# Kernel tuning notes

Hardware: AMD Instinct MI355X
Metric: run time of the kernel (lower is better)

## Reference

```python
import jax, jax.numpy as jnp
import numpy as np


def setup_inputs() -> dict:
    key = jax.random.key(0)
    ks = jax.random.split(key, 11)
    B, E, R, D = 2048, 20000, 500, 256
    inp = {
        "h": jax.random.uniform(ks[0], (B, E), dtype=jnp.float32),
        "t": jax.random.uniform(ks[1], (B, E), dtype=jnp.float32),
        "r": jax.random.uniform(ks[2], (B, R), dtype=jnp.float32),
        "W_er": jax.random.normal(ks[3], (D, E), dtype=jnp.float32) * 0.02,
        "W_ei": jax.random.normal(ks[4], (D, E), dtype=jnp.float32) * 0.02,
        "W_ej": jax.random.normal(ks[5], (D, E), dtype=jnp.float32) * 0.02,
        "W_ek": jax.random.normal(ks[6], (D, E), dtype=jnp.float32) * 0.02,
        "W_rr": jax.random.normal(ks[7], (D, R), dtype=jnp.float32) * 0.02,
        "W_ri": jax.random.normal(ks[8], (D, R), dtype=jnp.float32) * 0.02,
        "W_rj": jax.random.normal(ks[9], (D, R), dtype=jnp.float32) * 0.02,
        "W_rk": jax.random.normal(ks[10], (D, R), dtype=jnp.float32) * 0.02,
    }
    return inp


def reference(h, t, r, W_er, W_ei, W_ej, W_ek, W_rr, W_ri, W_rj, W_rk):
    # entity / relation projections (nn.Linear, no bias): x @ W^T -> [B, D]
    H_r, H_i, H_j, H_k = h @ W_er.T, h @ W_ei.T, h @ W_ej.T, h @ W_ek.T
    T_r, T_i, T_j, T_k = t @ W_er.T, t @ W_ei.T, t @ W_ej.T, t @ W_ek.T
    R_r, R_i, R_j, R_k = r @ W_rr.T, r @ W_ri.T, r @ W_rj.T, r @ W_rk.T

    # hypercomplex norm per row: sqrt(|R_r|^2 + |R_i|^2 + |R_j|^2 + |R_k|^2) -> [B,1]
    norm = jnp.sqrt(
        jnp.sum(R_r * R_r + R_i * R_i + R_j * R_j + R_k * R_k, axis=1, keepdims=True)
    )
    R_r, R_i, R_j, R_k = norm * R_r, norm * R_i, norm * R_j, norm * R_k

    # Hamilton product H (x) R
    Q_r = H_r * R_r - H_i * R_i - H_j * R_j - H_k * R_k
    Q_i = H_r * R_i + H_i * R_r + H_j * R_k - H_k * R_j
    Q_j = H_r * R_j - H_i * R_k + H_j * R_r + H_k * R_i
    Q_k = H_r * R_k + H_i * R_j - H_j * R_i + H_k * R_r

    # diag(Q @ T^T) == rowwise dot sum(Q*T, axis=1) -- O(B*d) form of the anti-pattern
    score = jnp.sum(Q_r * T_r + Q_i * T_i + Q_j * T_j + Q_k * T_k, axis=1, keepdims=True)
    return jax.nn.sigmoid(score)
```

## Files before the change

### kernel.cpp

```cpp
#include <hip/hip_runtime.h>


using bf16x8 = __attribute__((ext_vector_type(8))) short;
using f32x4  = __attribute__((ext_vector_type(4))) float;
using f32x16 = __attribute__((ext_vector_type(16))) float;

#define DEVINL static __device__ __forceinline__

DEVINL void split2(float x0, float x1, unsigned& h, unsigned& l) {
  unsigned u0 = __float_as_uint(x0), u1 = __float_as_uint(x1);
  unsigned h0 = u0 & 0xFFFF0000u, h1 = u1 & 0xFFFF0000u;
  h = (u0 >> 16) | h1;
  float r0 = x0 - __uint_as_float(h0);
  float r1 = x1 - __uint_as_float(h1);
  l = (__float_as_uint(r0) >> 16) | (__float_as_uint(r1) & 0xFFFF0000u);
}

DEVINL void gload16(const void* g, void* l) {
  __builtin_amdgcn_global_load_lds(
      (const __attribute__((address_space(1))) unsigned*)g,
      (__attribute__((address_space(3))) unsigned*)l, 16, 0, 0);
}

__global__ void convert_img(const float* __restrict__ src0,
                            const float* __restrict__ src1, int rows0,
                            int srcK, char* __restrict__ dst, int ktiles)
{
  const int kt = blockIdx.x, rt = blockIdx.y;
  const int m  = threadIdx.x;
  const int row = rt * 256 + m;
  const float* srow = (row < rows0) ? (src0 + (size_t)row * srcK)
                                    : (src1 + (size_t)(row - rows0) * srcK);
  char* base = dst + ((size_t)rt * ktiles + kt) * 32768
             + (m >> 5) * 2048 + (m & 31) * 16;
#pragma unroll
  for (int oct = 0; oct < 4; ++oct) {
    int k0 = kt * 32 + oct * 8;
    float x[8];
    if (k0 + 8 <= srcK) {
      float4 v0 = *(const float4*)(srow + k0);
      float4 v1 = *(const float4*)(srow + k0 + 4);
      x[0] = v0.x; x[1] = v0.y; x[2] = v0.z; x[3] = v0.w;
      x[4] = v1.x; x[5] = v1.y; x[6] = v1.z; x[7] = v1.w;
    } else {
#pragma unroll
      for (int j = 0; j < 8; ++j) x[j] = (k0 + j < srcK) ? srow[k0 + j] : 0.f;
    }
    unsigned hh[4], ll[4];
    split2(x[0], x[1], hh[0], ll[0]);
    split2(x[2], x[3], hh[1], ll[1]);
    split2(x[4], x[5], hh[2], ll[2]);
    split2(x[6], x[7], hh[3], ll[3]);
    int off = (oct >> 1) * 1024 + (oct & 1) * 512;
    *(uint4*)(base + off)         = make_uint4(hh[0], hh[1], hh[2], hh[3]);
    *(uint4*)(base + 16384 + off) = make_uint4(ll[0], ll[1], ll[2], ll[3]);
  }
}

__global__ __launch_bounds__(512, 2) void gemm_img(
    const char* __restrict__ Aimg, const char* __restrict__ Bimg, int ktiles,
    float* __restrict__ C, int MT, int NT, int KS, int swz)
{
  __shared__ __align__(16) char smem[131072];
  const int tid = threadIdx.x;
  const int bid = blockIdx.x;

  int mt, nt, ks;
  if (swz) {
    int x = bid & 7, w = bid >> 3;
    nt = w & 3;
    int g = x + (w >> 2) * 8;
    mt = g & 15; ks = g >> 4;
  } else {
    nt = bid % NT; int q = bid / NT; mt = q % MT; ks = q / MT;
  }

  const int kt0 = (ktiles * ks) / KS;
  const int kt1 = (ktiles * (ks + 1)) / KS;

  const char* Ab = Aimg + ((size_t)mt * ktiles + kt0) * 32768;
  const char* Bb = Bimg + ((size_t)nt * ktiles + kt0) * 32768;

  const int wid = tid >> 6, lane = tid & 63;
  const int wr = wid >> 2, wc = wid & 3;

  f32x16 acc[4][2];
#pragma unroll
  for (int mb = 0; mb < 4; ++mb)
#pragma unroll
    for (int nb = 0; nb < 2; ++nb)
#pragma unroll
      for (int e = 0; e < 16; ++e) acc[mb][nb][e] = 0.f;

  {
    const char* As = Ab + wid * 4096 + lane * 16;
    const char* Bs = Bb + wid * 4096 + lane * 16;
#pragma unroll
    for (int i = 0; i < 4; ++i) gload16(As + i * 1024, smem + wid * 4096 + i * 1024);
#pragma unroll
    for (int i = 0; i < 4; ++i) gload16(Bs + i * 1024, smem + 32768 + wid * 4096 + i * 1024);
  }
  asm volatile("s_waitcnt vmcnt(0)" ::: "memory");
  __builtin_amdgcn_s_barrier();

  for (int kt = kt0; kt < kt1; ++kt) {
    char* bufc = smem + (size_t)((kt - kt0) & 1) * 65536;
    char* bufn = smem + (size_t)(((kt - kt0) & 1) ^ 1) * 65536;
    const bool nx = (kt + 1 < kt1);

    if (nx) {
      const char* As = Ab + (size_t)(kt + 1 - kt0) * 32768 + wid * 4096 + lane * 16;
      const char* Bs = Bb + (size_t)(kt + 1 - kt0) * 32768 + wid * 4096 + lane * 16;
#pragma unroll
      for (int i = 0; i < 4; ++i) gload16(As + i * 1024, bufn + wid * 4096 + i * 1024);
#pragma unroll
      for (int i = 0; i < 4; ++i) gload16(Bs + i * 1024, bufn + 32768 + wid * 4096 + i * 1024);
    }

    bf16x8 bh[2][2], bl[2][2];
#pragma unroll
    for (int nb = 0; nb < 2; ++nb)
#pragma unroll
      for (int s = 0; s < 2; ++s) {
        const char* p = bufc + 32768 + (wc * 2 + nb) * 2048 + s * 1024 + lane * 16;
        bh[nb][s] = *(const bf16x8*)p;
        bl[nb][s] = *(const bf16x8*)(p + 16384);
      }

    __builtin_amdgcn_s_setprio(1);
#pragma unroll
    for (int mb = 0; mb < 4; ++mb) {
      const char* p = bufc + (wr * 4 + mb) * 2048 + lane * 16;
      bf16x8 ah0 = *(const bf16x8*)(p);
      bf16x8 al0 = *(const bf16x8*)(p + 16384);
      bf16x8 ah1 = *(const bf16x8*)(p + 1024);
      bf16x8 al1 = *(const bf16x8*)(p + 1024 + 16384);
#pragma unroll
      for (int nb = 0; nb < 2; ++nb) {
        f32x16* a = &acc[mb][nb];
        *a = __builtin_amdgcn_mfma_f32_32x32x16_bf16(ah0, bh[nb][0], *a, 0, 0, 0);
        *a = __builtin_amdgcn_mfma_f32_32x32x16_bf16(al0, bh[nb][0], *a, 0, 0, 0);
        *a = __builtin_amdgcn_mfma_f32_32x32x16_bf16(ah0, bl[nb][0], *a, 0, 0, 0);
        *a = __builtin_amdgcn_mfma_f32_32x32x16_bf16(ah1, bh[nb][1], *a, 0, 0, 0);
        *a = __builtin_amdgcn_mfma_f32_32x32x16_bf16(al1, bh[nb][1], *a, 0, 0, 0);
        *a = __builtin_amdgcn_mfma_f32_32x32x16_bf16(ah1, bl[nb][1], *a, 0, 0, 0);
      }
    }
    __builtin_amdgcn_s_setprio(0);

    asm volatile("s_waitcnt vmcnt(0)" ::: "memory");
    __builtin_amdgcn_s_barrier();
  }

  float* Cb = C + (size_t)ks * (size_t)(MT * 256) * 1024;
  const long rowbase = (long)mt * 256 + wr * 128 + 4 * (lane >> 5);
  const long colbase = (long)nt * 256 + wc * 64 + (lane & 31);
#pragma unroll
  for (int mb = 0; mb < 4; ++mb)
#pragma unroll
    for (int nb = 0; nb < 2; ++nb)
#pragma unroll
      for (int reg = 0; reg < 16; ++reg) {
        long row = rowbase + mb * 32 + (reg & 3) + 8 * (reg >> 2);
        long col = colbase + nb * 32;
        Cb[(size_t)row * 1024 + col] = acc[mb][nb][reg];
      }
}

__global__ void convert_b16(const float* __restrict__ src, int srcK,
                            char* __restrict__ dst)
{
  const int tile = blockIdx.x;
  const int wrow = threadIdx.x;
  char* base = dst + (size_t)tile * 32768;
  const float* srow = src + (size_t)wrow * srcK;
#pragma unroll
  for (int kc8 = 0; kc8 < 4; ++kc8) {
    int k0 = tile * 32 + kc8 * 8;
    float x[8];
    if (k0 + 8 <= srcK) {
      float4 v0 = *(const float4*)(srow + k0);
      float4 v1 = *(const float4*)(srow + k0 + 4);
      x[0] = v0.x; x[1] = v0.y; x[2] = v0.z; x[3] = v0.w;
      x[4] = v1.x; x[5] = v1.y; x[6] = v1.z; x[7] = v1.w;
    } else {
#pragma unroll
      for (int j = 0; j < 8; ++j) x[j] = (k0 + j < srcK) ? srow[k0 + j] : 0.f;
    }
    unsigned hh[4], ll[4];
    split2(x[0], x[1], hh[0], ll[0]);
    split2(x[2], x[3], hh[1], ll[1]);
    split2(x[4], x[5], hh[2], ll[2]);
    split2(x[6], x[7], hh[3], ll[3]);
    int lchunk = (wrow & 15) + kc8 * 16;
    int n16 = wrow >> 4;
    *(uint4*)(base + (size_t)n16 * 1024 + lchunk * 16)         = make_uint4(hh[0], hh[1], hh[2], hh[3]);
    *(uint4*)(base + 16384 + (size_t)n16 * 1024 + lchunk * 16) = make_uint4(ll[0], ll[1], ll[2], ll[3]);
  }
}

__global__ void pad_r(const float* __restrict__ src, float* __restrict__ dst)
{
  int row = blockIdx.y;
  int k = threadIdx.x * 4;
  float4 v = make_float4(0.f, 0.f, 0.f, 0.f);
  if (k + 3 < 500) v = *(const float4*)(src + (size_t)row * 500 + k);
  *(float4*)(dst + (size_t)row * 512 + k) = v;
}

__global__ __launch_bounds__(512, 2) void gemm3p(
    const float* __restrict__ A0, const float* __restrict__ A1, int mtA0, long lda,
    const char* __restrict__ Bimg, int ktilesTot,
    float* __restrict__ C, long ldc, int MT, int NT, int KS, int swz)
{
  extern __shared__ char smemd[];
  const int tid = threadIdx.x;
  const int bid = blockIdx.x;

  int mt, nt, ks;
  if (swz) {
    int x = bid & 7, w = bid >> 3;
    nt = w & 3;
    int g = x + (w >> 2) * 8;
    mt = g & 15; ks = g >> 4;
  } else {
    nt = bid % NT; int q = bid / NT; mt = q % MT; ks = q / MT;
  }

  const int kt0 = (ktilesTot * ks) / KS;
  const int kt1 = (ktilesTot * (ks + 1)) / KS;

  const float* Ablk = (mt < mtA0) ? (A0 + (size_t)mt * 256 * lda)
                                  : (A1 + (size_t)(mt - mtA0) * 256 * lda);
  const char* Bt = Bimg + ((size_t)nt * ktilesTot + kt0) * 32768;

  const int wid = tid >> 6, lane = tid & 63;
  const int wr = wid >> 2, wc = wid & 3;
  const int l15 = lane & 15, lq = lane >> 4;

  const float* aSrc = Ablk + (size_t)(wid * 32 + (lane >> 3)) * lda
                      + (size_t)kt0 * 32 + 4 * (lane & 7);

  int awoff[4];
  {
    int kg = (lane & 7) >> 1, half = lane & 1;
#pragma unroll
    for (int i = 0; i < 4; ++i) {
      int m15 = (lane >> 3) + 8 * (i & 1);
      awoff[i] = (2 * wid + (i >> 1)) * 2048 + (((m15 ^ kg) + kg * 16) << 4) + half * 8;
    }
  }
  const int aroff = (((l15 ^ lq) + lq * 16) << 4);
  const int bbase = 32768 + (wc * 4) * 1024 + lane * 16;

  f32x4 acc[8][4];
#pragma unroll
  for (int m = 0; m < 8; ++m)
#pragma unroll
    for (int j = 0; j < 4; ++j)
#pragma unroll
      for (int e = 0; e < 4; ++e) acc[m][j][e] = 0.f;

  float4 aR[4];

#define ISSUE_A(KT)                                                            \
  {                                                                            \
    const float* p_ = aSrc + (size_t)((KT) - kt0) * 32;                        \
    _Pragma("unroll")                                                          \
    for (int i = 0; i < 4; ++i) aR[i] = *(const float4*)(p_ + (size_t)(8 * i) * lda); \
  }
#define ISSUE_B(DST, KT)                                                       \
  {                                                                            \
    const char* p_ = Bt + (size_t)((KT) - kt0) * 32768 + wid * 4096 + lane * 16; \
    _Pragma("unroll")                                                          \
    for (int i = 0; i < 4; ++i)                                                \
      gload16(p_ + i * 1024, (DST) + 32768 + wid * 4096 + i * 1024);           \
  }
#define WRITE_A(DST)                                                           \
  {                                                                            \
    _Pragma("unroll")                                                          \
    for (int i = 0; i < 4; ++i) {                                              \
      unsigned h0_, l0_, h1_, l1_;                                             \
      split2(aR[i].x, aR[i].y, h0_, l0_);                                      \
      split2(aR[i].z, aR[i].w, h1_, l1_);                                      \
      *(uint2*)((DST) + awoff[i])        = make_uint2(h0_, h1_);               \
      *(uint2*)((DST) + awoff[i] + 1024) = make_uint2(l0_, l1_);               \
    }                                                                          \
  }

  ISSUE_A(kt0);
  ISSUE_B(smemd, kt0);
  WRITE_A(smemd);
  asm volatile("s_waitcnt vmcnt(0)" ::: "memory");
  asm volatile("s_waitcnt lgkmcnt(0)" ::: "memory");
  __builtin_amdgcn_s_barrier();

  for (int kt = kt0; kt < kt1; ++kt) {
    char* bufc = smemd + (size_t)((kt - kt0) & 1) * 65536;
    char* bufn = smemd + (size_t)(((kt - kt0) & 1) ^ 1) * 65536;
    const bool nx = (kt + 1 < kt1);

    if (nx) { ISSUE_A(kt + 1); ISSUE_B(bufn, kt + 1); }

    bf16x8 bh[4], bl[4];
#pragma unroll
    for (int j = 0; j < 4; ++j) {
      bh[j] = *(const bf16x8*)(bufc + bbase + j * 1024);
      bl[j] = *(const bf16x8*)(bufc + bbase + j * 1024 + 16384);
    }

    __builtin_amdgcn_s_setprio(1);
#pragma unroll
    for (int m = 0; m < 4; ++m) {
      const char* ab = bufc + (wr * 8 + m) * 2048;
      bf16x8 ah = *(const bf16x8*)(ab + aroff);
      bf16x8 al = *(const bf16x8*)(ab + aroff + 1024);
#pragma unroll
      for (int j = 0; j < 4; ++j) {
        acc[m][j] = __builtin_amdgcn_mfma_f32_16x16x32_bf16(ah, bh[j], acc[m][j], 0, 0, 0);
        acc[m][j] = __builtin_amdgcn_mfma_f32_16x16x32_bf16(al, bh[j], acc[m][j], 0, 0, 0);
        acc[m][j] = __builtin_amdgcn_mfma_f32_16x16x32_bf16(ah, bl[j], acc[m][j], 0, 0, 0);
      }
    }
    __builtin_amdgcn_s_setprio(0);

    __builtin_amdgcn_sched_barrier(0);
    if (nx) WRITE_A(bufn);

    __builtin_amdgcn_s_setprio(1);
#pragma unroll
    for (int m = 4; m < 8; ++m) {
      const char* ab = bufc + (wr * 8 + m) * 2048;
      bf16x8 ah = *(const bf16x8*)(ab + aroff);
      bf16x8 al = *(const bf16x8*)(ab + aroff + 1024);
#pragma unroll
      for (int j = 0; j < 4; ++j) {
        acc[m][j] = __builtin_amdgcn_mfma_f32_16x16x32_bf16(ah, bh[j], acc[m][j], 0, 0, 0);
        acc[m][j] = __builtin_amdgcn_mfma_f32_16x16x32_bf16(al, bh[j], acc[m][j], 0, 0, 0);
        acc[m][j] = __builtin_amdgcn_mfma_f32_16x16x32_bf16(ah, bl[j], acc[m][j], 0, 0, 0);
      }
    }
    __builtin_amdgcn_s_setprio(0);

    asm volatile("s_waitcnt vmcnt(0)" ::: "memory");
    asm volatile("s_waitcnt lgkmcnt(0)" ::: "memory");
    __builtin_amdgcn_s_barrier();
  }
#undef ISSUE_A
#undef ISSUE_B
#undef WRITE_A

  float* Cb = C + (size_t)ks * (size_t)(MT * 256) * (size_t)ldc;
  const long rowbase = (long)mt * 256 + wr * 128 + lq * 4;
  const long colbase = (long)nt * 256 + wc * 64 + l15;
#pragma unroll
  for (int m = 0; m < 8; ++m)
#pragma unroll
    for (int j = 0; j < 4; ++j)
#pragma unroll
      for (int reg = 0; reg < 4; ++reg) {
        long row = rowbase + m * 16 + reg;
        long col = colbase + j * 16;
        Cb[(size_t)row * ldc + col] = acc[m][j][reg];
      }
}

__global__ void epilogue_kernel(const float* __restrict__ C1, const float* __restrict__ C2,
                                float* __restrict__ out, int KS)
{
  const int b = blockIdx.x;
  const int d = threadIdx.x;
  const size_t SZ = 4096ull * 1024ull;

  float Hq[4], Tq[4], Rq[4];
#pragma unroll
  for (int q = 0; q < 4; ++q) {
    float hv = 0.f, tv = 0.f;
    for (int ks = 0; ks < KS; ++ks) {
      hv += C1[ks * SZ + (size_t)b * 1024 + q * 256 + d];
      tv += C1[ks * SZ + (size_t)(b + 2048) * 1024 + q * 256 + d];
    }
    Hq[q] = hv; Tq[q] = tv;
    Rq[q] = C2[(size_t)b * 1024 + q * 256 + d];
  }
  float nn = Rq[0]*Rq[0] + Rq[1]*Rq[1] + Rq[2]*Rq[2] + Rq[3]*Rq[3];
  float Qr = Hq[0]*Rq[0] - Hq[1]*Rq[1] - Hq[2]*Rq[2] - Hq[3]*Rq[3];
  float Qi = Hq[0]*Rq[1] + Hq[1]*Rq[0] + Hq[2]*Rq[3] - Hq[3]*Rq[2];
  float Qj = Hq[0]*Rq[2] - Hq[1]*Rq[3] + Hq[2]*Rq[0] + Hq[3]*Rq[1];
  float Qk = Hq[0]*Rq[3] + Hq[1]*Rq[2] - Hq[2]*Rq[1] + Hq[3]*Rq[0];
  float ss = Qr*Tq[0] + Qi*Tq[1] + Qj*Tq[2] + Qk*Tq[3];

#pragma unroll
  for (int o = 32; o; o >>= 1) {
    ss += __shfl_xor(ss, o);
    nn += __shfl_xor(nn, o);
  }
  __shared__ float red[8];
  int lane = d & 63, w = d >> 6;
  if (lane == 0) { red[w] = ss; red[4 + w] = nn; }
  __syncthreads();
  if (d == 0) {
    float S = red[0] + red[1] + red[2] + red[3];
    float N = red[4] + red[5] + red[6] + red[7];
    float score = sqrtf(N) * S;
    out[b] = 1.f / (1.f + expf(-score));
  }
}

extern "C" void kernel_launch(void* const* d_in, const int* in_sizes, int n_in,
                              void* d_out, int out_size, void* d_ws, size_t ws_size,
                              hipStream_t stream)
{
  const float* h = (const float*)d_in[0];
  const float* t = (const float*)d_in[1];
  const float* r = (const float*)d_in[2];
  const float* We[4] = {(const float*)d_in[3], (const float*)d_in[4],
                        (const float*)d_in[5], (const float*)d_in[6]};
  const float* Wr[4] = {(const float*)d_in[7], (const float*)d_in[8],
                        (const float*)d_in[9], (const float*)d_in[10]};
  float* out = (float*)d_out;
  char* ws = (char*)d_ws;

  const size_t offA  = 0;
  const size_t offB  = 327680000;
  const size_t offWr = offB + 81920000;
  const size_t offRi = offWr + 2097152;
  const size_t offC1 = offRi + 4194304;
  const size_t C1sz  = 4096ull * 1024ull * 4ull;
  const size_t offC2 = offC1 + 4 * C1sz;
  const size_t needImg = offC2 + 8388608;

  if (ws_size >= needImg) {
    float* C1 = (float*)(ws + offC1);
    float* C2 = (float*)(ws + offC2);

    convert_img<<<dim3(625, 16), 256, 0, stream>>>(h, t, 2048, 20000, ws + offA, 625);
    for (int q = 0; q < 4; ++q) {
      convert_img<<<dim3(625, 1), 256, 0, stream>>>(
          We[q], We[q], 2048, 20000, ws + offB + (size_t)q * 625 * 32768, 625);
      convert_img<<<dim3(16, 1), 256, 0, stream>>>(
          Wr[q], Wr[q], 2048, 500, ws + offWr + (size_t)q * 16 * 32768, 16);
    }
    convert_img<<<dim3(16, 8), 256, 0, stream>>>(r, r, 4096, 500, ws + offRi, 16);

    gemm_img<<<dim3(256), 512, 0, stream>>>(
        ws + offA, ws + offB, 625, C1, 16, 4, 4, 1);
    gemm_img<<<dim3(32), 512, 0, stream>>>(
        ws + offRi, ws + offWr, 16, C2, 8, 4, 1, 0);

    epilogue_kernel<<<dim3(2048), 256, 0, stream>>>(C1, C2, out, 4);
    return;
  }

  const size_t fB  = 0;
  const size_t fWr = 81920000;
  const size_t fR  = fWr + 2097152;
  const size_t fC1 = fR + 4194304;
  const int KS = (ws_size >= fC1 + 4 * C1sz + 8388608ull) ? 4 : 2;
  const size_t fC2 = fC1 + (size_t)KS * C1sz;

  float* rpad = (float*)(ws + fR);
  float* C1   = (float*)(ws + fC1);
  float* C2   = (float*)(ws + fC2);

  for (int q = 0; q < 4; ++q) {
    convert_b16<<<dim3(625), 256, 0, stream>>>(We[q], 20000, ws + fB + (size_t)q * 625 * 32768);
    convert_b16<<<dim3(16), 256, 0, stream>>>(Wr[q], 500, ws + fWr + (size_t)q * 16 * 32768);
  }
  pad_r<<<dim3(1, 2048), 128, 0, stream>>>(r, rpad);

  gemm3p<<<dim3(16 * 4 * KS), 512, 131072, stream>>>(
      h, t, 8, 20000L, (const char*)(ws + fB), 625,
      C1, 1024L, 16, 4, KS, KS == 4 ? 1 : 0);
  gemm3p<<<dim3(32), 512, 131072, stream>>>(
      rpad, rpad, 8, 512L, (const char*)(ws + fWr), 16,
      C2, 1024L, 8, 4, 1, 0);

  epilogue_kernel<<<dim3(2048), 256, 0, stream>>>(C1, C2, out, KS);
}
```

Before: 690.1 us.

## Switch GEMM to 128-row tiles with single-buffered LDS and 4 waves

Rewrites the split-bf16 GEMM kernel to use 128x256 output tiles with 256 threads and a single 64KB LDS buffer instead of 256x256 tiles with 512 threads and double buffering. The convert kernel is parameterised by row tile so the A image matches the 128-row layout, and the grid grows to 512 blocks. It also prefetches A fragments from LDS ahead of the MFMA loop with sched barriers. The aims are more blocks for occupancy and lower LDS per block, at the cost of no global-load/compute overlap and less data reuse per tile.

```diff
diff --git a/kernel.cpp b/kernel.cpp
--- a/kernel.cpp
+++ b/kernel.cpp
@@ -24,14 +24,17 @@
 
 __global__ void convert_img(const float* __restrict__ src0,
                             const float* __restrict__ src1, int rows0,
-                            int srcK, char* __restrict__ dst, int ktiles)
+                            int srcK, char* __restrict__ dst, int ktiles,
+                            int rtile)
 {
   const int kt = blockIdx.x, rt = blockIdx.y;
   const int m  = threadIdx.x;
-  const int row = rt * 256 + m;
+  const int row = rt * rtile + m;
   const float* srow = (row < rows0) ? (src0 + (size_t)row * srcK)
                                     : (src1 + (size_t)(row - rows0) * srcK);
-  char* base = dst + ((size_t)rt * ktiles + kt) * 32768
+  const size_t tileB = (size_t)rtile * 128;
+  const int plane = rtile * 64;
+  char* base = dst + ((size_t)rt * ktiles + kt) * tileB
              + (m >> 5) * 2048 + (m & 31) * 16;
 #pragma unroll
   for (int oct = 0; oct < 4; ++oct) {
@@ -53,36 +56,33 @@
     split2(x[6], x[7], hh[3], ll[3]);
     int off = (oct >> 1) * 1024 + (oct & 1) * 512;
     *(uint4*)(base + off)         = make_uint4(hh[0], hh[1], hh[2], hh[3]);
-    *(uint4*)(base + 16384 + off) = make_uint4(ll[0], ll[1], ll[2], ll[3]);
-  }
-}
-
-__global__ __launch_bounds__(512, 2) void gemm_img(
+    *(uint4*)(base + plane + off) = make_uint4(ll[0], ll[1], ll[2], ll[3]);
+  }
+}
+
+__global__ __launch_bounds__(256, 2) void gemm_sb(
     const char* __restrict__ Aimg, const char* __restrict__ Bimg, int ktiles,
     float* __restrict__ C, int MT, int NT, int KS, int swz)
 {
-  __shared__ __align__(16) char smem[131072];
-  const int tid = threadIdx.x;
+  __shared__ __align__(16) char smem[65536];
   const int bid = blockIdx.x;
 
   int mt, nt, ks;
   if (swz) {
-    int x = bid & 7, w = bid >> 3;
-    nt = w & 3;
-    int g = x + (w >> 2) * 8;
-    mt = g & 15; ks = g >> 4;
+    int x = bid & 7, i = bid >> 3;
+    nt = x & 3;
+    int u = (x >> 2) + 2 * i;
+    mt = u >> 2; ks = u & 3;
   } else {
     nt = bid % NT; int q = bid / NT; mt = q % MT; ks = q / MT;
   }
 
-  const int kt0 = (ktiles * ks) / KS;
-  const int kt1 = (ktiles * (ks + 1)) / KS;
-
-  const char* Ab = Aimg + ((size_t)mt * ktiles + kt0) * 32768;
+  const int kt0 = (ktiles * ks) / KS, kt1 = (ktiles * (ks + 1)) / KS;
+  const char* Ab = Aimg + ((size_t)mt * ktiles + kt0) * 16384;
   const char* Bb = Bimg + ((size_t)nt * ktiles + kt0) * 32768;
 
-  const int wid = tid >> 6, lane = tid & 63;
-  const int wr = wid >> 2, wc = wid & 3;
+  const int wid = threadIdx.x >> 6, lane = threadIdx.x & 63;
+  const int wc = wid;
 
   f32x16 acc[4][2];
 #pragma unroll
@@ -92,68 +92,67 @@
 #pragma unroll
       for (int e = 0; e < 16; ++e) acc[mb][nb][e] = 0.f;
 
-  {
-    const char* As = Ab + wid * 4096 + lane * 16;
-    const char* Bs = Bb + wid * 4096 + lane * 16;
-#pragma unroll
-    for (int i = 0; i < 4; ++i) gload16(As + i * 1024, smem + wid * 4096 + i * 1024);
-#pragma unroll
-    for (int i = 0; i < 4; ++i) gload16(Bs + i * 1024, smem + 32768 + wid * 4096 + i * 1024);
-  }
-  asm volatile("s_waitcnt vmcnt(0)" ::: "memory");
-  __builtin_amdgcn_s_barrier();
-
   for (int kt = kt0; kt < kt1; ++kt) {
-    char* bufc = smem + (size_t)((kt - kt0) & 1) * 65536;
-    char* bufn = smem + (size_t)(((kt - kt0) & 1) ^ 1) * 65536;
-    const bool nx = (kt + 1 < kt1);
-
-    if (nx) {
-      const char* As = Ab + (size_t)(kt + 1 - kt0) * 32768 + wid * 4096 + lane * 16;
-      const char* Bs = Bb + (size_t)(kt + 1 - kt0) * 32768 + wid * 4096 + lane * 16;
-#pragma unroll
-      for (int i = 0; i < 4; ++i) gload16(As + i * 1024, bufn + wid * 4096 + i * 1024);
-#pragma unroll
-      for (int i = 0; i < 4; ++i) gload16(Bs + i * 1024, bufn + 32768 + wid * 4096 + i * 1024);
-    }
+    {
+      const char* As = Ab + (size_t)(kt - kt0) * 16384 + wid * 4096 + lane * 16;
+#pragma unroll
+      for (int i = 0; i < 4; ++i)
+        gload16(As + i * 1024, smem + wid * 4096 + i * 1024);
+      const char* Bs = Bb + (size_t)(kt - kt0) * 32768 + wid * 8192 + lane * 16;
+#pragma unroll
+      for (int i = 0; i < 8; ++i)
+        gload16(Bs + i * 1024, smem + 16384 + wid * 8192 + i * 1024);
+    }
+    asm volatile("s_waitcnt vmcnt(0)" ::: "memory");
+    __builtin_amdgcn_s_barrier();
 
     bf16x8 bh[2][2], bl[2][2];
 #pragma unroll
     for (int nb = 0; nb < 2; ++nb)
 #pragma unroll
       for (int s = 0; s < 2; ++s) {
-        const char* p = bufc + 32768 + (wc * 2 + nb) * 2048 + s * 1024 + lane * 16;
+        const char* p = smem + 16384 + (wc * 2 + nb) * 2048 + s * 1024 + lane * 16;
         bh[nb][s] = *(const bf16x8*)p;
         bl[nb][s] = *(const bf16x8*)(p + 16384);
       }
-
-    __builtin_amdgcn_s_setprio(1);
+    bf16x8 ah[4][2], al[4][2];
+#pragma unroll
+    for (int mb = 0; mb < 2; ++mb)
+#pragma unroll
+      for (int s = 0; s < 2; ++s) {
+        const char* p = smem + mb * 2048 + s * 1024 + lane * 16;
+        ah[mb][s] = *(const bf16x8*)p;
+        al[mb][s] = *(const bf16x8*)(p + 8192);
+      }
 #pragma unroll
     for (int mb = 0; mb < 4; ++mb) {
-      const char* p = bufc + (wr * 4 + mb) * 2048 + lane * 16;
-      bf16x8 ah0 = *(const bf16x8*)(p);
-      bf16x8 al0 = *(const bf16x8*)(p + 16384);
-      bf16x8 ah1 = *(const bf16x8*)(p + 1024);
-      bf16x8 al1 = *(const bf16x8*)(p + 1024 + 16384);
-#pragma unroll
-      for (int nb = 0; nb < 2; ++nb) {
-        f32x16* a = &acc[mb][nb];
-        *a = __builtin_amdgcn_mfma_f32_32x32x16_bf16(ah0, bh[nb][0], *a, 0, 0, 0);
-        *a = __builtin_amdgcn_mfma_f32_32x32x16_bf16(al0, bh[nb][0], *a, 0, 0, 0);
-        *a = __builtin_amdgcn_mfma_f32_32x32x16_bf16(ah0, bl[nb][0], *a, 0, 0, 0);
-        *a = __builtin_amdgcn_mfma_f32_32x32x16_bf16(ah1, bh[nb][1], *a, 0, 0, 0);
-        *a = __builtin_amdgcn_mfma_f32_32x32x16_bf16(al1, bh[nb][1], *a, 0, 0, 0);
-        *a = __builtin_amdgcn_mfma_f32_32x32x16_bf16(ah1, bl[nb][1], *a, 0, 0, 0);
-      }
-    }
-    __builtin_amdgcn_s_setprio(0);
-
-    asm volatile("s_waitcnt vmcnt(0)" ::: "memory");
+      if (mb < 2) {
+#pragma unroll
+        for (int s = 0; s < 2; ++s) {
+          const char* p = smem + (mb + 2) * 2048 + s * 1024 + lane * 16;
+          ah[mb + 2][s] = *(const bf16x8*)p;
+          al[mb + 2][s] = *(const bf16x8*)(p + 8192);
+        }
+      }
+      __builtin_amdgcn_sched_barrier(0);
+      __builtin_amdgcn_s_setprio(1);
+#pragma unroll
+      for (int nb = 0; nb < 2; ++nb)
+#pragma unroll
+        for (int s = 0; s < 2; ++s) {
+          f32x16* a = &acc[mb][nb];
+          *a = __builtin_amdgcn_mfma_f32_32x32x16_bf16(ah[mb][s], bh[nb][s], *a, 0, 0, 0);
+          *a = __builtin_amdgcn_mfma_f32_32x32x16_bf16(al[mb][s], bh[nb][s], *a, 0, 0, 0);
+          *a = __builtin_amdgcn_mfma_f32_32x32x16_bf16(ah[mb][s], bl[nb][s], *a, 0, 0, 0);
+        }
+      __builtin_amdgcn_s_setprio(0);
+      __builtin_amdgcn_sched_barrier(0);
+    }
     __builtin_amdgcn_s_barrier();
   }
 
-  float* Cb = C + (size_t)ks * (size_t)(MT * 256) * 1024;
-  const long rowbase = (long)mt * 256 + wr * 128 + 4 * (lane >> 5);
+  float* Cb = C + (size_t)ks * (size_t)(MT * 128) * 1024;
+  const long rowbase = (long)mt * 128 + 4 * (lane >> 5);
   const long colbase = (long)nt * 256 + wc * 64 + (lane & 31);
 #pragma unroll
   for (int mb = 0; mb < 4; ++mb)
@@ -434,19 +433,19 @@
     float* C1 = (float*)(ws + offC1);
     float* C2 = (float*)(ws + offC2);
 
-    convert_img<<<dim3(625, 16), 256, 0, stream>>>(h, t, 2048, 20000, ws + offA, 625);
+    convert_img<<<dim3(625, 32), 128, 0, stream>>>(h, t, 2048, 20000, ws + offA, 625, 128);
     for (int q = 0; q < 4; ++q) {
       convert_img<<<dim3(625, 1), 256, 0, stream>>>(
-          We[q], We[q], 2048, 20000, ws + offB + (size_t)q * 625 * 32768, 625);
+          We[q], We[q], 2048, 20000, ws + offB + (size_t)q * 625 * 32768, 625, 256);
       convert_img<<<dim3(16, 1), 256, 0, stream>>>(
-          Wr[q], Wr[q], 2048, 500, ws + offWr + (size_t)q * 16 * 32768, 16);
-    }
-    convert_img<<<dim3(16, 8), 256, 0, stream>>>(r, r, 4096, 500, ws + offRi, 16);
-
-    gemm_img<<<dim3(256), 512, 0, stream>>>(
-        ws + offA, ws + offB, 625, C1, 16, 4, 4, 1);
-    gemm_img<<<dim3(32), 512, 0, stream>>>(
-        ws + offRi, ws + offWr, 16, C2, 8, 4, 1, 0);
+          Wr[q], Wr[q], 2048, 500, ws + offWr + (size_t)q * 16 * 32768, 16, 256);
+    }
+    convert_img<<<dim3(16, 16), 128, 0, stream>>>(r, r, 2048, 500, ws + offRi, 16, 128);
+
+    gemm_sb<<<dim3(512), 256, 0, stream>>>(
+        ws + offA, ws + offB, 625, C1, 32, 4, 4, 1);
+    gemm_sb<<<dim3(64), 256, 0, stream>>>(
+        ws + offRi, ws + offWr, 16, C2, 16, 4, 1, 0);
 
     epilogue_kernel<<<dim3(2048), 256, 0, stream>>>(C1, C2, out, 4);
     return;
```

Result: slower. 732.1 us (+6.1%).

## Load GEMM operands directly from global into registers and stage conversion via LDS

Applied to the files above, without the earlier changes.

The GEMM kernel stops staging A/B tiles through double-buffered LDS with async global-to-LDS loads. Each wave now loads its fragments straight from the pre-swizzled image into registers, with software pipelining across B sub-blocks and the next k-tile. Wave tiling changes from 2x4 to 4x2 waves, so each wave covers 64x128. The convert kernel is rewritten to use coalesced row reads into LDS before splitting and writing hi/lo bf16, with smaller 64-row blocks. The aim is to remove LDS traffic and barriers from the main loop, at the cost of redundant global/L2 reads across waves and more register pressure.

```diff
diff --git a/kernel.cpp b/kernel.cpp
--- a/kernel.cpp
+++ b/kernel.cpp
@@ -22,47 +22,61 @@
       (__attribute__((address_space(3))) unsigned*)l, 16, 0, 0);
 }
 
-__global__ void convert_img(const float* __restrict__ src0,
-                            const float* __restrict__ src1, int rows0,
-                            int srcK, char* __restrict__ dst, int ktiles)
-{
-  const int kt = blockIdx.x, rt = blockIdx.y;
-  const int m  = threadIdx.x;
-  const int row = rt * 256 + m;
-  const float* srow = (row < rows0) ? (src0 + (size_t)row * srcK)
-                                    : (src1 + (size_t)(row - rows0) * srcK);
-  char* base = dst + ((size_t)rt * ktiles + kt) * 32768
-             + (m >> 5) * 2048 + (m & 31) * 16;
-#pragma unroll
-  for (int oct = 0; oct < 4; ++oct) {
-    int k0 = kt * 32 + oct * 8;
+__global__ void convert_img2(const float* __restrict__ src0,
+                             const float* __restrict__ src1, int rows0,
+                             int srcK, char* __restrict__ dst, int ktiles)
+{
+  __shared__ float ld[64][36];
+  const int kt = blockIdx.x, rb = blockIdx.y;
+  const int t = threadIdx.x;
+
+  {
+    int r = t >> 2, kc = (t & 3) * 8;
+    int row = rb * 64 + r;
+    const float* srow = (row < rows0) ? (src0 + (size_t)row * srcK)
+                                      : (src1 + (size_t)(row - rows0) * srcK);
+    int k0 = kt * 32 + kc;
+    float4 v0, v1;
+    if (k0 + 8 <= srcK) {
+      v0 = *(const float4*)(srow + k0);
+      v1 = *(const float4*)(srow + k0 + 4);
+    } else {
+      float x[8];
+#pragma unroll
+      for (int j = 0; j < 8; ++j) x[j] = (k0 + j < srcK) ? srow[k0 + j] : 0.f;
+      v0 = make_float4(x[0], x[1], x[2], x[3]);
+      v1 = make_float4(x[4], x[5], x[6], x[7]);
+    }
+    *(float4*)&ld[r][kc]     = v0;
+    *(float4*)&ld[r][kc + 4] = v1;
+  }
+  __syncthreads();
+
+  {
+    int g = t >> 7, s = (t >> 6) & 1, kh = (t >> 5) & 1, r31 = t & 31;
+    int row = g * 32 + r31;
+    int k = s * 16 + kh * 8;
     float x[8];
-    if (k0 + 8 <= srcK) {
-      float4 v0 = *(const float4*)(srow + k0);
-      float4 v1 = *(const float4*)(srow + k0 + 4);
-      x[0] = v0.x; x[1] = v0.y; x[2] = v0.z; x[3] = v0.w;
-      x[4] = v1.x; x[5] = v1.y; x[6] = v1.z; x[7] = v1.w;
-    } else {
-#pragma unroll
-      for (int j = 0; j < 8; ++j) x[j] = (k0 + j < srcK) ? srow[k0 + j] : 0.f;
-    }
-    unsigned hh[4], ll[4];
-    split2(x[0], x[1], hh[0], ll[0]);
-    split2(x[2], x[3], hh[1], ll[1]);
-    split2(x[4], x[5], hh[2], ll[2]);
-    split2(x[6], x[7], hh[3], ll[3]);
-    int off = (oct >> 1) * 1024 + (oct & 1) * 512;
-    *(uint4*)(base + off)         = make_uint4(hh[0], hh[1], hh[2], hh[3]);
-    *(uint4*)(base + 16384 + off) = make_uint4(ll[0], ll[1], ll[2], ll[3]);
-  }
-}
-
-__global__ __launch_bounds__(512, 2) void gemm_img(
+#pragma unroll
+    for (int j = 0; j < 8; ++j) x[j] = ld[row][k + j];
+    unsigned hh[4], llv[4];
+    split2(x[0], x[1], hh[0], llv[0]);
+    split2(x[2], x[3], hh[1], llv[1]);
+    split2(x[4], x[5], hh[2], llv[2]);
+    split2(x[6], x[7], hh[3], llv[3]);
+    int tile_rt = rb >> 2;
+    int gbase = (rb & 3) * 2;
+    char* base = dst + ((size_t)tile_rt * ktiles + kt) * 32768
+               + (gbase + g) * 2048 + s * 1024 + kh * 512 + r31 * 16;
+    *(uint4*)base           = make_uint4(hh[0], hh[1], hh[2], hh[3]);
+    *(uint4*)(base + 16384) = make_uint4(llv[0], llv[1], llv[2], llv[3]);
+  }
+}
+
+__global__ __launch_bounds__(512, 2) void gemm_dir(
     const char* __restrict__ Aimg, const char* __restrict__ Bimg, int ktiles,
     float* __restrict__ C, int MT, int NT, int KS, int swz)
 {
-  __shared__ __align__(16) char smem[131072];
-  const int tid = threadIdx.x;
   const int bid = blockIdx.x;
 
   int mt, nt, ks;
@@ -78,87 +92,98 @@
   const int kt0 = (ktiles * ks) / KS;
   const int kt1 = (ktiles * (ks + 1)) / KS;
 
-  const char* Ab = Aimg + ((size_t)mt * ktiles + kt0) * 32768;
-  const char* Bb = Bimg + ((size_t)nt * ktiles + kt0) * 32768;
-
-  const int wid = tid >> 6, lane = tid & 63;
-  const int wr = wid >> 2, wc = wid & 3;
-
-  f32x16 acc[4][2];
-#pragma unroll
-  for (int mb = 0; mb < 4; ++mb)
-#pragma unroll
-    for (int nb = 0; nb < 2; ++nb)
+  const char* Akt = Aimg + ((size_t)mt * ktiles + kt0) * 32768;
+  const char* Bkt = Bimg + ((size_t)nt * ktiles + kt0) * 32768;
+
+  const int wid = threadIdx.x >> 6, lane = threadIdx.x & 63;
+  const int wr = wid >> 1, wc = wid & 1;
+
+  const int aoff = wr * 2 * 2048 + lane * 16;
+  const int boff = wc * 4 * 2048 + lane * 16;
+
+  f32x16 acc[2][4];
+#pragma unroll
+  for (int mb = 0; mb < 2; ++mb)
+#pragma unroll
+    for (int nb = 0; nb < 4; ++nb)
 #pragma unroll
       for (int e = 0; e < 16; ++e) acc[mb][nb][e] = 0.f;
 
-  {
-    const char* As = Ab + wid * 4096 + lane * 16;
-    const char* Bs = Bb + wid * 4096 + lane * 16;
-#pragma unroll
-    for (int i = 0; i < 4; ++i) gload16(As + i * 1024, smem + wid * 4096 + i * 1024);
-#pragma unroll
-    for (int i = 0; i < 4; ++i) gload16(Bs + i * 1024, smem + 32768 + wid * 4096 + i * 1024);
-  }
-  asm volatile("s_waitcnt vmcnt(0)" ::: "memory");
-  __builtin_amdgcn_s_barrier();
-
-  for (int kt = kt0; kt < kt1; ++kt) {
-    char* bufc = smem + (size_t)((kt - kt0) & 1) * 65536;
-    char* bufn = smem + (size_t)(((kt - kt0) & 1) ^ 1) * 65536;
-    const bool nx = (kt + 1 < kt1);
-
-    if (nx) {
-      const char* As = Ab + (size_t)(kt + 1 - kt0) * 32768 + wid * 4096 + lane * 16;
-      const char* Bs = Bb + (size_t)(kt + 1 - kt0) * 32768 + wid * 4096 + lane * 16;
-#pragma unroll
-      for (int i = 0; i < 4; ++i) gload16(As + i * 1024, bufn + wid * 4096 + i * 1024);
-#pragma unroll
-      for (int i = 0; i < 4; ++i) gload16(Bs + i * 1024, bufn + 32768 + wid * 4096 + i * 1024);
-    }
-
-    bf16x8 bh[2][2], bl[2][2];
-#pragma unroll
-    for (int nb = 0; nb < 2; ++nb)
-#pragma unroll
-      for (int s = 0; s < 2; ++s) {
-        const char* p = bufc + 32768 + (wc * 2 + nb) * 2048 + s * 1024 + lane * 16;
-        bh[nb][s] = *(const bf16x8*)p;
-        bl[nb][s] = *(const bf16x8*)(p + 16384);
-      }
-
-    __builtin_amdgcn_s_setprio(1);
-#pragma unroll
-    for (int mb = 0; mb < 4; ++mb) {
-      const char* p = bufc + (wr * 4 + mb) * 2048 + lane * 16;
-      bf16x8 ah0 = *(const bf16x8*)(p);
-      bf16x8 al0 = *(const bf16x8*)(p + 16384);
-      bf16x8 ah1 = *(const bf16x8*)(p + 1024);
-      bf16x8 al1 = *(const bf16x8*)(p + 1024 + 16384);
-#pragma unroll
-      for (int nb = 0; nb < 2; ++nb) {
-        f32x16* a = &acc[mb][nb];
-        *a = __builtin_amdgcn_mfma_f32_32x32x16_bf16(ah0, bh[nb][0], *a, 0, 0, 0);
-        *a = __builtin_amdgcn_mfma_f32_32x32x16_bf16(al0, bh[nb][0], *a, 0, 0, 0);
-        *a = __builtin_amdgcn_mfma_f32_32x32x16_bf16(ah0, bl[nb][0], *a, 0, 0, 0);
-        *a = __builtin_amdgcn_mfma_f32_32x32x16_bf16(ah1, bh[nb][1], *a, 0, 0, 0);
-        *a = __builtin_amdgcn_mfma_f32_32x32x16_bf16(al1, bh[nb][1], *a, 0, 0, 0);
-        *a = __builtin_amdgcn_mfma_f32_32x32x16_bf16(ah1, bl[nb][1], *a, 0, 0, 0);
-      }
-    }
-    __builtin_amdgcn_s_setprio(0);
-
-    asm volatile("s_waitcnt vmcnt(0)" ::: "memory");
-    __builtin_amdgcn_s_barrier();
-  }
+  bf16x8 aA[8], aB[8];
+  bf16x8 bb[2][4];
+
+#define LDA(DST, BASE)                                                         \
+  {                                                                            \
+    _Pragma("unroll")                                                          \
+    for (int mb = 0; mb < 2; ++mb)                                             \
+      _Pragma("unroll")                                                        \
+      for (int s = 0; s < 2; ++s)                                              \
+        _Pragma("unroll")                                                      \
+        for (int pl = 0; pl < 2; ++pl)                                         \
+          (DST)[mb * 4 + s * 2 + pl] = *(const bf16x8*)((BASE) +               \
+              pl * 16384 + mb * 2048 + s * 1024 + aoff);                       \
+  }
+#define LDB(PAR, BASE, NB)                                                     \
+  {                                                                            \
+    _Pragma("unroll")                                                          \
+    for (int s = 0; s < 2; ++s)                                                \
+      _Pragma("unroll")                                                        \
+      for (int pl = 0; pl < 2; ++pl)                                           \
+        bb[PAR][s * 2 + pl] = *(const bf16x8*)((BASE) +                        \
+            pl * 16384 + (NB) * 2048 + s * 1024 + boff);                       \
+  }
+#define SB() __builtin_amdgcn_sched_barrier(0)
+#define CL(AC, PAR, NB)                                                        \
+  {                                                                            \
+    __builtin_amdgcn_s_setprio(1);                                             \
+    _Pragma("unroll")                                                          \
+    for (int mb = 0; mb < 2; ++mb)                                             \
+      _Pragma("unroll")                                                        \
+      for (int s = 0; s < 2; ++s) {                                            \
+        f32x16* a = &acc[mb][NB];                                              \
+        bf16x8 ah = (AC)[mb * 4 + s * 2 + 0];                                  \
+        bf16x8 al = (AC)[mb * 4 + s * 2 + 1];                                  \
+        bf16x8 bh = bb[PAR][s * 2 + 0];                                        \
+        bf16x8 bl = bb[PAR][s * 2 + 1];                                        \
+        *a = __builtin_amdgcn_mfma_f32_32x32x16_bf16(ah, bh, *a, 0, 0, 0);     \
+        *a = __builtin_amdgcn_mfma_f32_32x32x16_bf16(al, bh, *a, 0, 0, 0);     \
+        *a = __builtin_amdgcn_mfma_f32_32x32x16_bf16(ah, bl, *a, 0, 0, 0);     \
+      }                                                                        \
+    __builtin_amdgcn_s_setprio(0);                                             \
+  }
+#define TILE(AC, AN, NX)                                                       \
+  {                                                                            \
+    LDB(1, Bkt, 1);                        SB(); CL(AC, 0, 0); SB();           \
+    LDB(0, Bkt, 2);                        SB(); CL(AC, 1, 1); SB();           \
+    LDB(1, Bkt, 3);                                                            \
+    if (NX) LDA(AN, Akt + 32768);          SB(); CL(AC, 0, 2); SB();           \
+    if (NX) LDB(0, Bkt + 32768, 0);        SB(); CL(AC, 1, 3); SB();           \
+    Akt += 32768; Bkt += 32768;                                                \
+  }
+
+  LDA(aA, Akt);
+  LDB(0, Bkt, 0);
+  SB();
+
+  int kt = kt0;
+  for (; kt + 2 <= kt1; kt += 2) {
+    TILE(aA, aB, true);
+    TILE(aB, aA, (kt + 2) < kt1);
+  }
+  if (kt < kt1) TILE(aA, aB, false);
+#undef LDA
+#undef LDB
+#undef SB
+#undef CL
+#undef TILE
 
   float* Cb = C + (size_t)ks * (size_t)(MT * 256) * 1024;
-  const long rowbase = (long)mt * 256 + wr * 128 + 4 * (lane >> 5);
-  const long colbase = (long)nt * 256 + wc * 64 + (lane & 31);
-#pragma unroll
-  for (int mb = 0; mb < 4; ++mb)
-#pragma unroll
-    for (int nb = 0; nb < 2; ++nb)
+  const long rowbase = (long)mt * 256 + wr * 64 + 4 * (lane >> 5);
+  const long colbase = (long)nt * 256 + wc * 128 + (lane & 31);
+#pragma unroll
+  for (int mb = 0; mb < 2; ++mb)
+#pragma unroll
+    for (int nb = 0; nb < 4; ++nb)
 #pragma unroll
       for (int reg = 0; reg < 16; ++reg) {
         long row = rowbase + mb * 32 + (reg & 3) + 8 * (reg >> 2);
@@ -434,18 +459,18 @@
     float* C1 = (float*)(ws + offC1);
     float* C2 = (float*)(ws + offC2);
 
-    convert_img<<<dim3(625, 16), 256, 0, stream>>>(h, t, 2048, 20000, ws + offA, 625);
+    convert_img2<<<dim3(625, 64), 256, 0, stream>>>(h, t, 2048, 20000, ws + offA, 625);
     for (int q = 0; q < 4; ++q) {
-      convert_img<<<dim3(625, 1), 256, 0, stream>>>(
+      convert_img2<<<dim3(625, 4), 256, 0, stream>>>(
           We[q], We[q], 2048, 20000, ws + offB + (size_t)q * 625 * 32768, 625);
-      convert_img<<<dim3(16, 1), 256, 0, stream>>>(
+      convert_img2<<<dim3(16, 4), 256, 0, stream>>>(
           Wr[q], Wr[q], 2048, 500, ws + offWr + (size_t)q * 16 * 32768, 16);
     }
-    convert_img<<<dim3(16, 8), 256, 0, stream>>>(r, r, 4096, 500, ws + offRi, 16);
-
-    gemm_img<<<dim3(256), 512, 0, stream>>>(
+    convert_img2<<<dim3(16, 32), 256, 0, stream>>>(r, r, 2048, 500, ws + offRi, 16);
+
+    gemm_dir<<<dim3(256), 512, 0, stream>>>(
         ws + offA, ws + offB, 625, C1, 16, 4, 4, 1);
-    gemm_img<<<dim3(32), 512, 0, stream>>>(
+    gemm_dir<<<dim3(32), 512, 0, stream>>>(
         ws + offRi, ws + offWr, 16, C2, 8, 4, 1, 0);
 
     epilogue_kernel<<<dim3(2048), 256, 0, stream>>>(C1, C2, out, 4);
```

Measured after the change: 700.7 us. About the same (+1.5%).

## Shrink GEMM tiles to 128x128 with 2-way split-K and LDS-staged conversion

Applied to the files above, without the earlier changes.

The main GEMM drops from 256x256 tiles with 512 threads and 4-way split-K to 128x128 tiles with 256 threads and 2-way split-K, giving 512 blocks. This aims to improve load balance and occupancy, and it halves the partial-sum traffic through C1 and the epilogue. The conversion kernel now stages rows through shared memory so that global reads coalesce and it writes the new 128-row image layout. The MFMA loop is also reordered so that consecutive instructions go to independent accumulators. In exchange, each block reuses less data, so more operand bytes are loaded per FLOP.

```diff
diff --git a/kernel.cpp b/kernel.cpp
--- a/kernel.cpp
+++ b/kernel.cpp
@@ -22,55 +22,70 @@
       (__attribute__((address_space(3))) unsigned*)l, 16, 0, 0);
 }
 
-__global__ void convert_img(const float* __restrict__ src0,
-                            const float* __restrict__ src1, int rows0,
-                            int srcK, char* __restrict__ dst, int ktiles)
-{
-  const int kt = blockIdx.x, rt = blockIdx.y;
-  const int m  = threadIdx.x;
-  const int row = rt * 256 + m;
-  const float* srow = (row < rows0) ? (src0 + (size_t)row * srcK)
-                                    : (src1 + (size_t)(row - rows0) * srcK);
-  char* base = dst + ((size_t)rt * ktiles + kt) * 32768
-             + (m >> 5) * 2048 + (m & 31) * 16;
-#pragma unroll
-  for (int oct = 0; oct < 4; ++oct) {
-    int k0 = kt * 32 + oct * 8;
+__global__ void convert_img128(const float* __restrict__ src0,
+                               const float* __restrict__ src1, int rows0,
+                               int srcK, char* __restrict__ dst, int ktiles)
+{
+  __shared__ float ld[64][36];
+  const int kt = blockIdx.x, rb = blockIdx.y;
+  const int t = threadIdx.x;
+
+  {
+    int r = t >> 2, kc = (t & 3) * 8;
+    int row = rb * 64 + r;
+    const float* srow = (row < rows0) ? (src0 + (size_t)row * srcK)
+                                      : (src1 + (size_t)(row - rows0) * srcK);
+    int k0 = kt * 32 + kc;
+    float4 v0, v1;
+    if (k0 + 8 <= srcK) {
+      v0 = *(const float4*)(srow + k0);
+      v1 = *(const float4*)(srow + k0 + 4);
+    } else {
+      float x[8];
+#pragma unroll
+      for (int j = 0; j < 8; ++j) x[j] = (k0 + j < srcK) ? srow[k0 + j] : 0.f;
+      v0 = make_float4(x[0], x[1], x[2], x[3]);
+      v1 = make_float4(x[4], x[5], x[6], x[7]);
+    }
+    *(float4*)&ld[r][kc]     = v0;
+    *(float4*)&ld[r][kc + 4] = v1;
+  }
+  __syncthreads();
+
+  {
+    int g = t >> 7, s = (t >> 6) & 1, kh = (t >> 5) & 1, r31 = t & 31;
+    int row = g * 32 + r31;
+    int k = s * 16 + kh * 8;
     float x[8];
-    if (k0 + 8 <= srcK) {
-      float4 v0 = *(const float4*)(srow + k0);
-      float4 v1 = *(const float4*)(srow + k0 + 4);
-      x[0] = v0.x; x[1] = v0.y; x[2] = v0.z; x[3] = v0.w;
-      x[4] = v1.x; x[5] = v1.y; x[6] = v1.z; x[7] = v1.w;
-    } else {
-#pragma unroll
-      for (int j = 0; j < 8; ++j) x[j] = (k0 + j < srcK) ? srow[k0 + j] : 0.f;
-    }
-    unsigned hh[4], ll[4];
-    split2(x[0], x[1], hh[0], ll[0]);
-    split2(x[2], x[3], hh[1], ll[1]);
-    split2(x[4], x[5], hh[2], ll[2]);
-    split2(x[6], x[7], hh[3], ll[3]);
-    int off = (oct >> 1) * 1024 + (oct & 1) * 512;
-    *(uint4*)(base + off)         = make_uint4(hh[0], hh[1], hh[2], hh[3]);
-    *(uint4*)(base + 16384 + off) = make_uint4(ll[0], ll[1], ll[2], ll[3]);
-  }
-}
-
-__global__ __launch_bounds__(512, 2) void gemm_img(
+#pragma unroll
+    for (int j = 0; j < 8; ++j) x[j] = ld[row][k + j];
+    unsigned hh[4], llv[4];
+    split2(x[0], x[1], hh[0], llv[0]);
+    split2(x[2], x[3], hh[1], llv[1]);
+    split2(x[4], x[5], hh[2], llv[2]);
+    split2(x[6], x[7], hh[3], llv[3]);
+    int tile_rt = rb >> 1;
+    int gbase = (rb & 1) * 2;
+    char* base = dst + ((size_t)tile_rt * ktiles + kt) * 16384
+               + (gbase + g) * 2048 + s * 1024 + kh * 512 + r31 * 16;
+    *(uint4*)base          = make_uint4(hh[0], hh[1], hh[2], hh[3]);
+    *(uint4*)(base + 8192) = make_uint4(llv[0], llv[1], llv[2], llv[3]);
+  }
+}
+
+__global__ __launch_bounds__(256, 2) void gemm_t128(
     const char* __restrict__ Aimg, const char* __restrict__ Bimg, int ktiles,
     float* __restrict__ C, int MT, int NT, int KS, int swz)
 {
-  __shared__ __align__(16) char smem[131072];
-  const int tid = threadIdx.x;
+  __shared__ __align__(16) char smem[65536];
   const int bid = blockIdx.x;
 
   int mt, nt, ks;
   if (swz) {
-    int x = bid & 7, w = bid >> 3;
-    nt = w & 3;
-    int g = x + (w >> 2) * 8;
-    mt = g & 15; ks = g >> 4;
+    int x = bid & 7, i = bid >> 3;
+    nt = i & 7;
+    int P = x * 8 + (i >> 3);
+    ks = P & 1; mt = P >> 1;
   } else {
     nt = bid % NT; int q = bid / NT; mt = q % MT; ks = q / MT;
   }
@@ -78,15 +93,15 @@
   const int kt0 = (ktiles * ks) / KS;
   const int kt1 = (ktiles * (ks + 1)) / KS;
 
-  const char* Ab = Aimg + ((size_t)mt * ktiles + kt0) * 32768;
-  const char* Bb = Bimg + ((size_t)nt * ktiles + kt0) * 32768;
-
-  const int wid = tid >> 6, lane = tid & 63;
-  const int wr = wid >> 2, wc = wid & 3;
-
-  f32x16 acc[4][2];
-#pragma unroll
-  for (int mb = 0; mb < 4; ++mb)
+  const char* Ab = Aimg + ((size_t)mt * ktiles + kt0) * 16384;
+  const char* Bb = Bimg + ((size_t)nt * ktiles + kt0) * 16384;
+
+  const int wid = threadIdx.x >> 6, lane = threadIdx.x & 63;
+  const int wr = wid >> 1, wc = wid & 1;
+
+  f32x16 acc[2][2];
+#pragma unroll
+  for (int mb = 0; mb < 2; ++mb)
 #pragma unroll
     for (int nb = 0; nb < 2; ++nb)
 #pragma unroll
@@ -98,65 +113,67 @@
 #pragma unroll
     for (int i = 0; i < 4; ++i) gload16(As + i * 1024, smem + wid * 4096 + i * 1024);
 #pragma unroll
-    for (int i = 0; i < 4; ++i) gload16(Bs + i * 1024, smem + 32768 + wid * 4096 + i * 1024);
+    for (int i = 0; i < 4; ++i) gload16(Bs + i * 1024, smem + 16384 + wid * 4096 + i * 1024);
   }
   asm volatile("s_waitcnt vmcnt(0)" ::: "memory");
   __builtin_amdgcn_s_barrier();
 
   for (int kt = kt0; kt < kt1; ++kt) {
-    char* bufc = smem + (size_t)((kt - kt0) & 1) * 65536;
-    char* bufn = smem + (size_t)(((kt - kt0) & 1) ^ 1) * 65536;
+    char* bufc = smem + (size_t)((kt - kt0) & 1) * 32768;
+    char* bufn = smem + (size_t)(((kt - kt0) & 1) ^ 1) * 32768;
     const bool nx = (kt + 1 < kt1);
 
     if (nx) {
-      const char* As = Ab + (size_t)(kt + 1 - kt0) * 32768 + wid * 4096 + lane * 16;
-      const char* Bs = Bb + (size_t)(kt + 1 - kt0) * 32768 + wid * 4096 + lane * 16;
+      const char* As = Ab + (size_t)(kt + 1 - kt0) * 16384 + wid * 4096 + lane * 16;
+      const char* Bs = Bb + (size_t)(kt + 1 - kt0) * 16384 + wid * 4096 + lane * 16;
 #pragma unroll
       for (int i = 0; i < 4; ++i) gload16(As + i * 1024, bufn + wid * 4096 + i * 1024);
 #pragma unroll
-      for (int i = 0; i < 4; ++i) gload16(Bs + i * 1024, bufn + 32768 + wid * 4096 + i * 1024);
-    }
-
-    bf16x8 bh[2][2], bl[2][2];
+      for (int i = 0; i < 4; ++i) gload16(Bs + i * 1024, bufn + 16384 + wid * 4096 + i * 1024);
+    }
+
+    bf16x8 ah[2][2], al[2][2], bh[2][2], bl[2][2];
+#pragma unroll
+    for (int mb = 0; mb < 2; ++mb)
+#pragma unroll
+      for (int s = 0; s < 2; ++s) {
+        const char* p = bufc + (wr * 2 + mb) * 2048 + s * 1024 + lane * 16;
+        ah[mb][s] = *(const bf16x8*)p;
+        al[mb][s] = *(const bf16x8*)(p + 8192);
+      }
 #pragma unroll
     for (int nb = 0; nb < 2; ++nb)
 #pragma unroll
       for (int s = 0; s < 2; ++s) {
-        const char* p = bufc + 32768 + (wc * 2 + nb) * 2048 + s * 1024 + lane * 16;
+        const char* p = bufc + 16384 + (wc * 2 + nb) * 2048 + s * 1024 + lane * 16;
         bh[nb][s] = *(const bf16x8*)p;
-        bl[nb][s] = *(const bf16x8*)(p + 16384);
+        bl[nb][s] = *(const bf16x8*)(p + 8192);
       }
 
     __builtin_amdgcn_s_setprio(1);
 #pragma unroll
-    for (int mb = 0; mb < 4; ++mb) {
-      const char* p = bufc + (wr * 4 + mb) * 2048 + lane * 16;
-      bf16x8 ah0 = *(const bf16x8*)(p);
-      bf16x8 al0 = *(const bf16x8*)(p + 16384);
-      bf16x8 ah1 = *(const bf16x8*)(p + 1024);
-      bf16x8 al1 = *(const bf16x8*)(p + 1024 + 16384);
-#pragma unroll
-      for (int nb = 0; nb < 2; ++nb) {
-        f32x16* a = &acc[mb][nb];
-        *a = __builtin_amdgcn_mfma_f32_32x32x16_bf16(ah0, bh[nb][0], *a, 0, 0, 0);
-        *a = __builtin_amdgcn_mfma_f32_32x32x16_bf16(al0, bh[nb][0], *a, 0, 0, 0);
-        *a = __builtin_amdgcn_mfma_f32_32x32x16_bf16(ah0, bl[nb][0], *a, 0, 0, 0);
-        *a = __builtin_amdgcn_mfma_f32_32x32x16_bf16(ah1, bh[nb][1], *a, 0, 0, 0);
-        *a = __builtin_amdgcn_mfma_f32_32x32x16_bf16(al1, bh[nb][1], *a, 0, 0, 0);
-        *a = __builtin_amdgcn_mfma_f32_32x32x16_bf16(ah1, bl[nb][1], *a, 0, 0, 0);
-      }
-    }
+    for (int p = 0; p < 3; ++p)
+#pragma unroll
+      for (int s = 0; s < 2; ++s)
+#pragma unroll
+        for (int mb = 0; mb < 2; ++mb)
+#pragma unroll
+          for (int nb = 0; nb < 2; ++nb) {
+            bf16x8 av = (p == 1) ? al[mb][s] : ah[mb][s];
+            bf16x8 bv = (p == 2) ? bl[nb][s] : bh[nb][s];
+            acc[mb][nb] = __builtin_amdgcn_mfma_f32_32x32x16_bf16(av, bv, acc[mb][nb], 0, 0, 0);
+          }
     __builtin_amdgcn_s_setprio(0);
 
     asm volatile("s_waitcnt vmcnt(0)" ::: "memory");
     __builtin_amdgcn_s_barrier();
   }
 
-  float* Cb = C + (size_t)ks * (size_t)(MT * 256) * 1024;
-  const long rowbase = (long)mt * 256 + wr * 128 + 4 * (lane >> 5);
-  const long colbase = (long)nt * 256 + wc * 64 + (lane & 31);
-#pragma unroll
-  for (int mb = 0; mb < 4; ++mb)
+  float* Cb = C + (size_t)ks * (size_t)(MT * 128) * 1024;
+  const long rowbase = (long)mt * 128 + wr * 64 + 4 * (lane >> 5);
+  const long colbase = (long)nt * 128 + wc * 64 + (lane & 31);
+#pragma unroll
+  for (int mb = 0; mb < 2; ++mb)
 #pragma unroll
     for (int nb = 0; nb < 2; ++nb)
 #pragma unroll
@@ -427,28 +444,28 @@
   const size_t offRi = offWr + 2097152;
   const size_t offC1 = offRi + 4194304;
   const size_t C1sz  = 4096ull * 1024ull * 4ull;
-  const size_t offC2 = offC1 + 4 * C1sz;
+  const size_t offC2 = offC1 + 2 * C1sz;
   const size_t needImg = offC2 + 8388608;
 
   if (ws_size >= needImg) {
     float* C1 = (float*)(ws + offC1);
     float* C2 = (float*)(ws + offC2);
 
-    convert_img<<<dim3(625, 16), 256, 0, stream>>>(h, t, 2048, 20000, ws + offA, 625);
+    convert_img128<<<dim3(625, 64), 256, 0, stream>>>(h, t, 2048, 20000, ws + offA, 625);
     for (int q = 0; q < 4; ++q) {
-      convert_img<<<dim3(625, 1), 256, 0, stream>>>(
-          We[q], We[q], 2048, 20000, ws + offB + (size_t)q * 625 * 32768, 625);
-      convert_img<<<dim3(16, 1), 256, 0, stream>>>(
-          Wr[q], Wr[q], 2048, 500, ws + offWr + (size_t)q * 16 * 32768, 16);
-    }
-    convert_img<<<dim3(16, 8), 256, 0, stream>>>(r, r, 4096, 500, ws + offRi, 16);
-
-    gemm_img<<<dim3(256), 512, 0, stream>>>(
-        ws + offA, ws + offB, 625, C1, 16, 4, 4, 1);
-    gemm_img<<<dim3(32), 512, 0, stream>>>(
-        ws + offRi, ws + offWr, 16, C2, 8, 4, 1, 0);
-
-    epilogue_kernel<<<dim3(2048), 256, 0, stream>>>(C1, C2, out, 4);
+      convert_img128<<<dim3(625, 4), 256, 0, stream>>>(
+          We[q], We[q], 2048, 20000, ws + offB + (size_t)q * 2 * 625 * 16384, 625);
+      convert_img128<<<dim3(16, 4), 256, 0, stream>>>(
+          Wr[q], Wr[q], 2048, 500, ws + offWr + (size_t)q * 2 * 16 * 16384, 16);
+    }
+    convert_img128<<<dim3(16, 32), 256, 0, stream>>>(r, r, 2048, 500, ws + offRi, 16);
+
+    gemm_t128<<<dim3(512), 256, 0, stream>>>(
+        ws + offA, ws + offB, 625, C1, 32, 8, 2, 1);
+    gemm_t128<<<dim3(128), 256, 0, stream>>>(
+        ws + offRi, ws + offWr, 16, C2, 16, 8, 1, 0);
+
+    epilogue_kernel<<<dim3(2048), 256, 0, stream>>>(C1, C2, out, 2);
     return;
   }
 
```

Measured after the change: 616.1 us. 10.7% less time.
